# Kernel optimization log

Measured on AMD Instinct MI355X. Metric: run time of the kernel, lower is better.

Reference implementation:

```python
import jax, jax.numpy as jnp
import numpy as np

N = 100000      # nodes (categories_nums[0])
E = 1600000     # edges
FEAT = 16       # features_num
HID = 32        # hidden
IDE = 16        # id_embed_size
EMB = 8         # embed_size
CAT_MAX = 1000  # categorical vocab (categories_nums[1:])
K = 3           # TAGConv hops (sparse=False)
NC = 2          # num_class
IN_DIM = IDE + 2 * EMB + HID  # 64 -> TAGConv input
EPS = 1e-5


def layer_norm(x, g, b):
    m = jnp.mean(x, axis=-1, keepdims=True)
    v = jnp.mean((x - m) ** 2, axis=-1, keepdims=True)
    return (x - m) * jax.lax.rsqrt(v + EPS) * g + b


def setup_inputs() -> dict:
    key = jax.random.key(0)
    ks = jax.random.split(key, 20)
    s = 0.05
    return {
        "x": jax.random.normal(ks[0], (N, FEAT), jnp.float32),
        "edge_index": jax.random.randint(ks[1], (2, E), 0, N, jnp.int64),
        "edge_weight": jax.random.uniform(ks[2], (E,), jnp.float32),
        "categories_value": jax.random.randint(ks[3], (N, 3), 0, CAT_MAX, jnp.int64),
        "id_table": jax.random.normal(ks[4], (N, IDE), jnp.float32) * s,
        "lin0_id_W": jax.random.normal(ks[5], (IDE, IDE), jnp.float32) * s,
        "lin0_id_b": jnp.zeros((IDE,), jnp.float32),
        "emb1": jax.random.normal(ks[6], (CAT_MAX, EMB), jnp.float32) * s,
        "emb2": jax.random.normal(ks[7], (CAT_MAX, EMB), jnp.float32) * s,
        "lin0_emb_W": jax.random.normal(ks[8], (2 * EMB, 2 * EMB), jnp.float32) * s,
        "lin0_emb_b": jnp.zeros((2 * EMB,), jnp.float32),
        "lin0_W": jax.random.normal(ks[9], (FEAT, HID), jnp.float32) * s,
        "lin0_b": jnp.zeros((HID,), jnp.float32),
        "ln0_g": jnp.ones((IN_DIM,), jnp.float32),
        "ln0_b": jnp.zeros((IN_DIM,), jnp.float32),
        "tag_W": jax.random.normal(ks[10], (K + 1, IN_DIM, HID), jnp.float32) * s,
        "tag_b": jnp.zeros((HID,), jnp.float32),
        "ln1_g": jnp.ones((HID,), jnp.float32),
        "ln1_b": jnp.zeros((HID,), jnp.float32),
        "lin1_W": jax.random.normal(ks[11], (HID, NC), jnp.float32) * s,
        "lin1_b": jnp.zeros((NC,), jnp.float32),
    }


def reference(x, edge_index, edge_weight, categories_value, id_table, lin0_id_W,
              lin0_id_b, emb1, emb2, lin0_emb_W, lin0_emb_b, lin0_W, lin0_b,
              ln0_g, ln0_b, tag_W, tag_b, ln1_g, ln1_b, lin1_W, lin1_b):
    # eval mode: dropouts are identity
    h = jax.nn.elu(x @ lin0_W + lin0_b)                       # [N, HID]
    ide = id_table[categories_value[:, 0]]                    # [N, IDE]
    ide = jax.nn.elu(ide @ lin0_id_W + lin0_id_b)
    er = jnp.concatenate([emb1[categories_value[:, 1]],
                          emb2[categories_value[:, 2]]], axis=1)  # [N, 2*EMB]
    er = jax.nn.elu(er @ lin0_emb_W + lin0_emb_b)
    feat = jnp.concatenate([ide, h, er], axis=1)              # [N, IN_DIM]
    feat = layer_norm(feat, ln0_g, ln0_b)

    # TAGConv: gcn_norm without self-loops, K-hop propagation
    row, col = edge_index[0], edge_index[1]                   # source -> target
    deg = jax.ops.segment_sum(edge_weight, col, num_segments=N)
    dis = jnp.where(deg > 0, deg ** -0.5, 0.0)
    norm = dis[row] * edge_weight * dis[col]                  # [E]

    out = feat @ tag_W[0]                                     # [N, HID]
    xk = feat
    for k in range(1, K + 1):
        xk = jax.ops.segment_sum(xk[row] * norm[:, None], col, num_segments=N)
        out = out + xk @ tag_W[k]
    out = out + tag_b

    out = jax.nn.relu(out)
    out = layer_norm(out, ln1_g, ln1_b)
    out = out @ lin1_W + lin1_b                               # [N, NC]
    return jax.nn.log_softmax(out, axis=-1)
```

## Files before the change

kernel.cpp:

```cpp
#include <hip/hip_runtime.h>
#include <hip/hip_bf16.h>

typedef unsigned short u16;
typedef unsigned int   u32;
typedef unsigned long long u64;
typedef u32 u32x2 __attribute__((ext_vector_type(2)));
typedef u32 u32x4 __attribute__((ext_vector_type(4)));

#define FIX_SCALE 16777216.0f
#define FIX_INV   (1.0f / 16777216.0f)
#define CNT_SHIFT 40
#define DEG_MASK  ((1ULL << CNT_SHIFT) - 1)

__device__ __forceinline__ float b2f(u16 u) { return __uint_as_float(((u32)u) << 16); }
__device__ __forceinline__ u16 f2b(float f) {
    u32 u = __float_as_uint(f);
    return (u16)((u + 0x7FFFu + ((u >> 16) & 1u)) >> 16);
}
__device__ __forceinline__ float elu(float v) { return v > 0.f ? v : expm1f(v); }
__device__ __forceinline__ float ldf(const void* p, size_t i, int f32) {
    return f32 ? ((const float*)p)[i] : b2f(((const u16*)p)[i]);
}
__device__ __forceinline__ float plo(u32 a) { return __uint_as_float(a << 16); }
__device__ __forceinline__ float phi(u32 a) { return __uint_as_float(a & 0xFFFF0000u); }

__global__ void k_flags(const u32* __restrict__ gw, const int* __restrict__ ei,
                        const int* __restrict__ cat, int* __restrict__ flags) {
    if (threadIdx.x == 0 && blockIdx.x == 0) {
        flags[0] = (gw[0] == 0x3F800000u) ? 1 : 0;
        flags[1] = ((ei[1]  | ei[3]  | ei[5]  | ei[7])  == 0) ? 2 : 1;
        flags[2] = ((cat[1] | cat[3] | cat[5] | cat[7]) == 0) ? 2 : 1;
    }
}

__global__ __launch_bounds__(256) void k_feathist(
    const void* __restrict__ x, const int* __restrict__ cat,
    const void* __restrict__ id_table, const void* __restrict__ W_id, const void* __restrict__ b_id,
    const void* __restrict__ emb1, const void* __restrict__ emb2,
    const void* __restrict__ W_emb, const void* __restrict__ b_emb,
    const void* __restrict__ W0, const void* __restrict__ b0,
    const void* __restrict__ g0, const void* __restrict__ bb0,
    const void* __restrict__ tagW0,
    u32* __restrict__ feat, float* __restrict__ out_acc,
    const int* __restrict__ ei, const void* __restrict__ ew,
    u64* __restrict__ packed, u16* __restrict__ rank,
    const int* __restrict__ flags, int N, int E, int nbN)
{
    __shared__ float sW0[512];
    __shared__ float sb0[32];
    __shared__ float sWid[256];
    __shared__ float sbid[16];
    __shared__ float sWe[256];
    __shared__ float sbe[16];
    __shared__ float sg[64], sb[64];
    __shared__ float sT0t[2048];
    int tid = threadIdx.x;
    int f32 = flags[0], s = flags[1], cs = flags[2];

    int e0 = blockIdx.x * 512 + tid;
    int e1 = e0 + 256;
    u64 old0 = 0, old1 = 0;
    bool h0 = (e0 < E), h1 = (e1 < E);
    const int* colp = ei + (size_t)E * s;
    if (h0) {
        int cdst = colp[(size_t)e0 * s];
        float w = ldf(ew, e0, f32);
        old0 = atomicAdd(&packed[cdst], (1ULL << CNT_SHIFT) | (u64)(w * FIX_SCALE + 0.5f));
    }
    if (h1) {
        int cdst = colp[(size_t)e1 * s];
        float w = ldf(ew, e1, f32);
        old1 = atomicAdd(&packed[cdst], (1ULL << CNT_SHIFT) | (u64)(w * FIX_SCALE + 0.5f));
    }

    if (blockIdx.x < nbN) {
        for (int i = tid; i < 512; i += 256) sW0[i] = ldf(W0, i, f32);
        if (tid < 32) sb0[tid] = ldf(b0, tid, f32);
        sWid[tid] = ldf(W_id, tid, f32);
        if (tid < 16) sbid[tid] = ldf(b_id, tid, f32);
        sWe[tid] = ldf(W_emb, tid, f32);
        if (tid < 16) sbe[tid] = ldf(b_emb, tid, f32);
        if (tid < 64) { sg[tid] = ldf(g0, tid, f32); sb[tid] = ldf(bb0, tid, f32); }
        for (int i = tid; i < 2048; i += 256) {
            int j = i >> 6, d = i & 63;
            sT0t[i] = ldf(tagW0, (size_t)d * 32 + j, f32);
        }
        __syncthreads();

        int i = blockIdx.x * 256 + tid;
        if (i < N) {
            size_t cb = (size_t)i * 3 * cs;
            int c0 = cat[cb], c1 = cat[cb + cs], c2 = cat[cb + 2 * cs];
            float f[64];
            {
                float t[16];
                #pragma unroll
                for (int q = 0; q < 16; q++) t[q] = ldf(id_table, (size_t)c0 * 16 + q, f32);
                #pragma unroll
                for (int j = 0; j < 16; j++) {
                    float a = sbid[j];
                    #pragma unroll
                    for (int ff = 0; ff < 16; ff++) a += t[ff] * sWid[ff * 16 + j];
                    f[j] = elu(a);
                }
            }
            {
                float t[16];
                #pragma unroll
                for (int q = 0; q < 16; q++) t[q] = ldf(x, (size_t)i * 16 + q, f32);
                #pragma unroll
                for (int j = 0; j < 32; j++) {
                    float a = sb0[j];
                    #pragma unroll
                    for (int ff = 0; ff < 16; ff++) a += t[ff] * sW0[ff * 32 + j];
                    f[16 + j] = elu(a);
                }
            }
            {
                float t[16];
                #pragma unroll
                for (int q = 0; q < 8; q++) t[q] = ldf(emb1, (size_t)c1 * 8 + q, f32);
                #pragma unroll
                for (int q = 0; q < 8; q++) t[8 + q] = ldf(emb2, (size_t)c2 * 8 + q, f32);
                #pragma unroll
                for (int j = 0; j < 16; j++) {
                    float a = sbe[j];
                    #pragma unroll
                    for (int ff = 0; ff < 16; ff++) a += t[ff] * sWe[ff * 16 + j];
                    f[48 + j] = elu(a);
                }
            }
            float m = 0.f;
            #pragma unroll
            for (int d = 0; d < 64; d++) m += f[d];
            m *= (1.f / 64.f);
            float var = 0.f;
            #pragma unroll
            for (int d = 0; d < 64; d++) { float df = f[d] - m; var += df * df; }
            var *= (1.f / 64.f);
            float rs = rsqrtf(var + 1e-5f);
            #pragma unroll
            for (int d = 0; d < 64; d++) f[d] = (f[d] - m) * rs * sg[d] + sb[d];

            u32* fp = feat + (size_t)i * 32;
            #pragma unroll
            for (int q = 0; q < 32; q++) fp[q] = ((u32)f2b(f[2 * q + 1]) << 16) | f2b(f[2 * q]);

            float* oa = out_acc + (size_t)i * 32;
            for (int j = 0; j < 32; j++) {
                float a = 0.f;
                #pragma unroll
                for (int d = 0; d < 64; d++) a += f[d] * sT0t[j * 64 + d];
                oa[j] = a;
            }
        }
    }
    if (h0) rank[e0] = (u16)(old0 >> CNT_SHIFT);
    if (h1) rank[e1] = (u16)(old1 >> CNT_SHIFT);
}

__global__ __launch_bounds__(256) void k_scan1(const u64* __restrict__ packed, int* __restrict__ ebuf,
                                               int* __restrict__ bsum, float* __restrict__ dis, int N)
{
    __shared__ int sdat[256];
    int tid = threadIdx.x;
    int i = blockIdx.x * 256 + tid;
    u64 pv = (i < N) ? packed[i] : 0ULL;
    int v = (int)(pv >> CNT_SHIFT);
    sdat[tid] = v;
    __syncthreads();
    for (int off = 1; off < 256; off <<= 1) {
        int t = (tid >= off) ? sdat[tid - off] : 0;
        __syncthreads();
        sdat[tid] += t;
        __syncthreads();
    }
    if (i < N) {
        ebuf[i] = sdat[tid] - v;
        u64 db = pv & DEG_MASK;
        dis[i] = db ? rsqrtf((float)db * FIX_INV) : 0.f;
    }
    if (tid == 255) bsum[blockIdx.x] = sdat[255];
}

__global__ __launch_bounds__(512) void k_scan2(const int* __restrict__ bsum, int* __restrict__ boff, int NB)
{
    __shared__ int sdat[512];
    __shared__ int scarry;
    int tid = threadIdx.x;
    if (tid == 0) scarry = 0;
    __syncthreads();
    for (int base = 0; base < NB; base += 512) {
        int i = base + tid;
        int v = (i < NB) ? bsum[i] : 0;
        sdat[tid] = v;
        __syncthreads();
        for (int off = 1; off < 512; off <<= 1) {
            int t = (tid >= off) ? sdat[tid - off] : 0;
            __syncthreads();
            sdat[tid] += t;
            __syncthreads();
        }
        if (i < NB) boff[i] = scarry + sdat[tid] - v;
        __syncthreads();
        if (tid == 0) scarry += sdat[511];
        __syncthreads();
    }
}

__global__ __launch_bounds__(256) void k_scan3(const int* __restrict__ ebuf, const int* __restrict__ boff,
                                               int* __restrict__ rowptr, int N, int E)
{
    int i = blockIdx.x * 256 + threadIdx.x;
    if (i >= N) return;
    rowptr[i] = boff[blockIdx.x] + ebuf[i];
    if (i == N - 1) rowptr[N] = E;
}

__global__ __launch_bounds__(256) void k_scatter(const int* __restrict__ ei, const void* __restrict__ ew,
                                                 const float* __restrict__ dis, const u16* __restrict__ rank,
                                                 const int* __restrict__ rowptr, int2* __restrict__ csr,
                                                 const int* __restrict__ flags, int E)
{
    int f32 = flags[0], s = flags[1];
    const int* row = ei;
    const int* col = ei + (size_t)E * s;
    int e = blockIdx.x * 256 + threadIdx.x;
    if (e >= E) return;
    int r = row[(size_t)e * s], c = col[(size_t)e * s];
    float nrm = dis[r] * ldf(ew, e, f32) * dis[c];
    csr[rowptr[c] + (int)rank[e]] = make_int2(r, __float_as_int(nrm));
}

template<int FOLD>
__global__ __launch_bounds__(256) void k_hop(
    const u32* __restrict__ fin, u32* __restrict__ fout, float* __restrict__ oacc,
    const int* __restrict__ rowptr, const int2* __restrict__ csr,
    const void* __restrict__ tagW, const int* __restrict__ flags, int N, int k)
{
    __shared__ float sT[FOLD ? 2048 : 1];
    if (FOLD) {
        int f32 = flags[0];
        size_t tb = (size_t)k * 2048;
        for (int i = threadIdx.x; i < 2048; i += 256) sT[i] = ldf(tagW, tb + i, f32);
        __syncthreads();
    }
    int tid = threadIdx.x;
    int node = blockIdx.x * 4 + (tid >> 6);
    if (node >= N) return;
    int lane = tid & 63;
    int o = (lane >> 3) & 7;
    int c = lane & 7;
    int start = rowptr[node], end = rowptr[node + 1];

    const u32x4* fin4 = (const u32x4*)fin;
    float v0 = 0.f, v1 = 0.f, v2 = 0.f, v3 = 0.f;
    float v4 = 0.f, v5 = 0.f, v6 = 0.f, v7 = 0.f;
    int e = start;
    for (; e + 16 <= end; e += 16) {
        int2 ma = csr[e + o];
        int2 mb = csr[e + 8 + o];
        u32x4 aa = fin4[(size_t)(u32)ma.x * 8 + c];
        u32x4 ab = fin4[(size_t)(u32)mb.x * 8 + c];
        float wa = __int_as_float(ma.y), wb = __int_as_float(mb.y);
        v0 += plo(aa.x) * wa; v1 += phi(aa.x) * wa; v2 += plo(aa.y) * wa; v3 += phi(aa.y) * wa;
        v4 += plo(aa.z) * wa; v5 += phi(aa.z) * wa; v6 += plo(aa.w) * wa; v7 += phi(aa.w) * wa;
        v0 += plo(ab.x) * wb; v1 += phi(ab.x) * wb; v2 += plo(ab.y) * wb; v3 += phi(ab.y) * wb;
        v4 += plo(ab.z) * wb; v5 += phi(ab.z) * wb; v6 += plo(ab.w) * wb; v7 += phi(ab.w) * wb;
    }
    for (; e < end; e += 8) {
        int ee = e + o;
        int2 m = (ee < end) ? csr[ee] : make_int2(0, 0);
        u32x4 a = fin4[(size_t)(u32)m.x * 8 + c];
        float w = __int_as_float(m.y);
        v0 += plo(a.x) * w; v1 += phi(a.x) * w; v2 += plo(a.y) * w; v3 += phi(a.y) * w;
        v4 += plo(a.z) * w; v5 += phi(a.z) * w; v6 += plo(a.w) * w; v7 += phi(a.w) * w;
    }
    v0 += __shfl_xor(v0, 8);  v1 += __shfl_xor(v1, 8);  v2 += __shfl_xor(v2, 8);  v3 += __shfl_xor(v3, 8);
    v4 += __shfl_xor(v4, 8);  v5 += __shfl_xor(v5, 8);  v6 += __shfl_xor(v6, 8);  v7 += __shfl_xor(v7, 8);
    v0 += __shfl_xor(v0, 16); v1 += __shfl_xor(v1, 16); v2 += __shfl_xor(v2, 16); v3 += __shfl_xor(v3, 16);
    v4 += __shfl_xor(v4, 16); v5 += __shfl_xor(v5, 16); v6 += __shfl_xor(v6, 16); v7 += __shfl_xor(v7, 16);
    v0 += __shfl_xor(v0, 32); v1 += __shfl_xor(v1, 32); v2 += __shfl_xor(v2, 32); v3 += __shfl_xor(v3, 32);
    v4 += __shfl_xor(v4, 32); v5 += __shfl_xor(v5, 32); v6 += __shfl_xor(v6, 32); v7 += __shfl_xor(v7, 32);

    if (lane < 8) {
        u32x4 pw;
        pw.x = ((u32)f2b(v1) << 16) | f2b(v0);
        pw.y = ((u32)f2b(v3) << 16) | f2b(v2);
        pw.z = ((u32)f2b(v5) << 16) | f2b(v4);
        pw.w = ((u32)f2b(v7) << 16) | f2b(v6);
        ((u32x4*)fout)[(size_t)node * 8 + lane] = pw;
    }

    if (FOLD) {
        int col = lane & 31, h = lane >> 5;
        float acc = 0.f;
        #pragma unroll
        for (int q = 0; q < 4; q++) {
            int csrc = h * 4 + q;
            int d0 = csrc * 8;
            float b0 = __shfl(v0, csrc);
            float b1 = __shfl(v1, csrc);
            float b2 = __shfl(v2, csrc);
            float b3 = __shfl(v3, csrc);
            float b4 = __shfl(v4, csrc);
            float b5 = __shfl(v5, csrc);
            float b6 = __shfl(v6, csrc);
            float b7 = __shfl(v7, csrc);
            acc += b0 * sT[(d0 + 0) * 32 + col] + b1 * sT[(d0 + 1) * 32 + col]
                 + b2 * sT[(d0 + 2) * 32 + col] + b3 * sT[(d0 + 3) * 32 + col]
                 + b4 * sT[(d0 + 4) * 32 + col] + b5 * sT[(d0 + 5) * 32 + col]
                 + b6 * sT[(d0 + 6) * 32 + col] + b7 * sT[(d0 + 7) * 32 + col];
        }
        acc += __shfl_xor(acc, 32);
        if (h == 0) oacc[(size_t)node * 32 + col] += acc;
    }
}

__global__ __launch_bounds__(256) void k_head(
    const float* __restrict__ oacc, const u32* __restrict__ x2b, const u32* __restrict__ x3b,
    const void* __restrict__ tagW, const void* __restrict__ tag_b,
    const void* __restrict__ g1, const void* __restrict__ b1,
    const void* __restrict__ W1, const void* __restrict__ bb1,
    void* __restrict__ out, const int* __restrict__ flags, int N)
{
    __shared__ float sT2t[2048], sT3t[2048];
    __shared__ float stb[32], sg[32], sbb[32], sW1[64], sb1v[2];
    int tid = threadIdx.x;
    int f32 = flags[0];
    for (int i = tid; i < 2048; i += 256) {
        int j = i >> 6, d = i & 63;
        sT2t[i] = ldf(tagW, (size_t)2 * 2048 + (size_t)d * 32 + j, f32);
        sT3t[i] = ldf(tagW, (size_t)3 * 2048 + (size_t)d * 32 + j, f32);
    }
    if (tid < 32) { stb[tid] = ldf(tag_b, tid, f32); sg[tid] = ldf(g1, tid, f32); sbb[tid] = ldf(b1, tid, f32); }
    if (tid < 64) sW1[tid] = ldf(W1, tid, f32);
    if (tid < 2) sb1v[tid] = ldf(bb1, tid, f32);
    __syncthreads();

    int i = blockIdx.x * 256 + tid;
    if (i >= N) return;

    float acc[32];
    const float4* oa4 = (const float4*)(oacc + (size_t)i * 32);
    #pragma unroll
    for (int q = 0; q < 8; q++) {
        float4 t = oa4[q];
        acc[4 * q] = t.x; acc[4 * q + 1] = t.y; acc[4 * q + 2] = t.z; acc[4 * q + 3] = t.w;
    }
    float xv[64];
    {
        const u32* p = x2b + (size_t)i * 32;
        #pragma unroll
        for (int q = 0; q < 32; q++) { u32 a = p[q]; xv[2 * q] = plo(a); xv[2 * q + 1] = phi(a); }
        for (int j = 0; j < 32; j++) {
            float a = 0.f;
            #pragma unroll
            for (int d = 0; d < 64; d++) a += xv[d] * sT2t[j * 64 + d];
            acc[j] += a;
        }
    }
    {
        const u32* p = x3b + (size_t)i * 32;
        #pragma unroll
        for (int q = 0; q < 32; q++) { u32 a = p[q]; xv[2 * q] = plo(a); xv[2 * q + 1] = phi(a); }
        for (int j = 0; j < 32; j++) {
            float a = 0.f;
            #pragma unroll
            for (int d = 0; d < 64; d++) a += xv[d] * sT3t[j * 64 + d];
            acc[j] += a;
        }
    }
    float o[32]; float m = 0.f;
    #pragma unroll
    for (int j = 0; j < 32; j++) { float t = acc[j] + stb[j]; t = t > 0.f ? t : 0.f; o[j] = t; m += t; }
    m *= (1.f / 32.f);
    float var = 0.f;
    #pragma unroll
    for (int j = 0; j < 32; j++) { float d = o[j] - m; var += d * d; }
    var *= (1.f / 32.f);
    float rs = rsqrtf(var + 1e-5f);
    float z0 = sb1v[0], z1 = sb1v[1];
    #pragma unroll
    for (int j = 0; j < 32; j++) {
        float t = (o[j] - m) * rs * sg[j] + sbb[j];
        z0 += t * sW1[2 * j];
        z1 += t * sW1[2 * j + 1];
    }
    float mx = fmaxf(z0, z1);
    float l = mx + logf(expf(z0 - mx) + expf(z1 - mx));
    if (f32) {
        ((float*)out)[(size_t)i * 2]     = z0 - l;
        ((float*)out)[(size_t)i * 2 + 1] = z1 - l;
    } else {
        *((u32*)((u16*)out + (size_t)i * 2)) = ((u32)f2b(z1 - l) << 16) | f2b(z0 - l);
    }
}

extern "C" void kernel_launch(void* const* d_in, const int* in_sizes, int n_in,
                              void* d_out, int out_size, void* d_ws, size_t ws_size,
                              hipStream_t stream)
{
    const void* x        = d_in[0];
    const int*  ei       = (const int*)d_in[1];
    const void* ew       = d_in[2];
    const int*  cat      = (const int*)d_in[3];
    const void* id_table = d_in[4];
    const void* W_id     = d_in[5];
    const void* b_id     = d_in[6];
    const void* emb1     = d_in[7];
    const void* emb2     = d_in[8];
    const void* W_emb    = d_in[9];
    const void* b_emb    = d_in[10];
    const void* W0       = d_in[11];
    const void* b0       = d_in[12];
    const void* g0       = d_in[13];
    const void* bb0      = d_in[14];
    const void* tagW     = d_in[15];
    const void* tag_b    = d_in[16];
    const void* g1       = d_in[17];
    const void* b1       = d_in[18];
    const void* W1       = d_in[19];
    const void* bb1      = d_in[20];

    int N = in_sizes[0] / 16;
    int E = in_sizes[2];
    int nb = (N + 255) / 256;
    int eb = (E + 255) / 256;
    int eb2 = (E + 511) / 512;

    char* ws = (char*)d_ws;
    size_t off = 0;
    int*   flags  = (int*)(ws + off);   off += 256;
    float* oacc   = (float*)(ws + off); off += (size_t)N * 32 * 4;
    u32*   featA  = (u32*)(ws + off);   off += (size_t)N * 32 * 4;
    u32*   f1     = (u32*)(ws + off);   off += (size_t)N * 32 * 4;
    int2*  csr    = (int2*)(ws + off);  off += (size_t)E * 8;
    int*   rowptr = (int*)(ws + off);   off += ((size_t)N + 1) * 4;
    off = (off + 255) & ~(size_t)255;
    u16*   rank   = (u16*)(ws + off);   off += (size_t)E * 2;
    off = (off + 255) & ~(size_t)255;
    u64*   packed = (u64*)(ws + off);   off += (size_t)N * 8;
    int*   ebuf   = (int*)(ws + off);   off += (size_t)N * 4;
    float* dis    = (float*)(ws + off); off += (size_t)N * 4;
    int*   bsum   = (int*)(ws + off);   off += (size_t)nb * 4;
    int*   boff   = (int*)(ws + off);   off += (size_t)nb * 4;

    hipMemsetAsync(packed, 0, (size_t)N * 8, stream);
    k_flags<<<1, 64, 0, stream>>>((const u32*)g0, ei, cat, flags);

    k_feathist<<<eb2, 256, 0, stream>>>(x, cat, id_table, W_id, b_id, emb1, emb2, W_emb, b_emb,
                                        W0, b0, g0, bb0, tagW, featA, oacc,
                                        ei, ew, packed, rank, flags, N, E, nb);
    k_scan1<<<nb, 256, 0, stream>>>(packed, ebuf, bsum, dis, N);
    k_scan2<<<1, 512, 0, stream>>>(bsum, boff, nb);
    k_scan3<<<nb, 256, 0, stream>>>(ebuf, boff, rowptr, N, E);
    k_scatter<<<eb, 256, 0, stream>>>(ei, ew, dis, rank, rowptr, csr, flags, E);

    int hb = (N + 3) / 4;
    k_hop<1><<<hb, 256, 0, stream>>>(featA, f1, oacc, rowptr, csr, tagW, flags, N, 1);
    k_hop<0><<<hb, 256, 0, stream>>>(f1, featA, oacc, rowptr, csr, tagW, flags, N, 2);
    k_hop<0><<<hb, 256, 0, stream>>>(featA, f1, oacc, rowptr, csr, tagW, flags, N, 3);
    k_head<<<nb, 256, 0, stream>>>(oacc, featA, f1, tagW, tag_b, g1, b1, W1, bb1,
                                   d_out, flags, N);
}
```

Baseline: 434.0 us.

## Reassociate TAGConv with Horner form to propagate 32-wide projected features

Instead of propagating the 64-dim features three hops and projecting each hop, the feature kernel projects the normalized features by each tag weight up front (Z_k = feat·W_k, 32-wide). The hops then run in Horner form, A(A(A Z3 + Z2) + Z1), so every gather moves 32 bf16 values instead of 64 and the per-hop matmul folds disappear. This halves gather traffic in the hops and simplifies the head, at the cost of more matmul work and an 8192-float shared table in the feature kernel, which may lower its occupancy. It also changes where bf16 rounding happens.

Result: faster. 365.8 us (-15.7%).

```diff
diff --git a/kernel.cpp b/kernel.cpp
--- a/kernel.cpp
+++ b/kernel.cpp
@@ -40,8 +40,8 @@
     const void* __restrict__ W_emb, const void* __restrict__ b_emb,
     const void* __restrict__ W0, const void* __restrict__ b0,
     const void* __restrict__ g0, const void* __restrict__ bb0,
-    const void* __restrict__ tagW0,
-    u32* __restrict__ feat, float* __restrict__ out_acc,
+    const void* __restrict__ tagW,
+    float* __restrict__ out_acc, u32* __restrict__ z1, u32* __restrict__ z2, u32* __restrict__ z3,
     const int* __restrict__ ei, const void* __restrict__ ew,
     u64* __restrict__ packed, u16* __restrict__ rank,
     const int* __restrict__ flags, int N, int E, int nbN)
@@ -53,7 +53,7 @@
     __shared__ float sWe[256];
     __shared__ float sbe[16];
     __shared__ float sg[64], sb[64];
-    __shared__ float sT0t[2048];
+    __shared__ float sTt[8192];
     int tid = threadIdx.x;
     int f32 = flags[0], s = flags[1], cs = flags[2];
 
@@ -81,9 +81,9 @@
         sWe[tid] = ldf(W_emb, tid, f32);
         if (tid < 16) sbe[tid] = ldf(b_emb, tid, f32);
         if (tid < 64) { sg[tid] = ldf(g0, tid, f32); sb[tid] = ldf(bb0, tid, f32); }
-        for (int i = tid; i < 2048; i += 256) {
-            int j = i >> 6, d = i & 63;
-            sT0t[i] = ldf(tagW0, (size_t)d * 32 + j, f32);
+        for (int i = tid; i < 8192; i += 256) {
+            int k = i >> 11, r = i & 2047, j = r >> 6, d = r & 63;
+            sTt[i] = ldf(tagW, (size_t)k * 2048 + (size_t)d * 32 + j, f32);
         }
         __syncthreads();
 
@@ -142,16 +142,26 @@
             #pragma unroll
             for (int d = 0; d < 64; d++) f[d] = (f[d] - m) * rs * sg[d] + sb[d];
 
-            u32* fp = feat + (size_t)i * 32;
-            #pragma unroll
-            for (int q = 0; q < 32; q++) fp[q] = ((u32)f2b(f[2 * q + 1]) << 16) | f2b(f[2 * q]);
-
             float* oa = out_acc + (size_t)i * 32;
             for (int j = 0; j < 32; j++) {
                 float a = 0.f;
                 #pragma unroll
-                for (int d = 0; d < 64; d++) a += f[d] * sT0t[j * 64 + d];
+                for (int d = 0; d < 64; d++) a += f[d] * sTt[j * 64 + d];
                 oa[j] = a;
+            }
+            #pragma unroll
+            for (int k = 1; k <= 3; k++) {
+                u32* zp = ((k == 1) ? z1 : (k == 2) ? z2 : z3) + (size_t)i * 16;
+                const float* T = sTt + k * 2048;
+                for (int j = 0; j < 16; j++) {
+                    float a0 = 0.f, a1 = 0.f;
+                    #pragma unroll
+                    for (int d = 0; d < 64; d++) {
+                        a0 += f[d] * T[(2 * j) * 64 + d];
+                        a1 += f[d] * T[(2 * j + 1) * 64 + d];
+                    }
+                    zp[j] = ((u32)f2b(a1) << 16) | f2b(a0);
+                }
             }
         }
     }
@@ -232,19 +242,11 @@
     csr[rowptr[c] + (int)rank[e]] = make_int2(r, __float_as_int(nrm));
 }
 
-template<int FOLD>
-__global__ __launch_bounds__(256) void k_hop(
-    const u32* __restrict__ fin, u32* __restrict__ fout, float* __restrict__ oacc,
-    const int* __restrict__ rowptr, const int2* __restrict__ csr,
-    const void* __restrict__ tagW, const int* __restrict__ flags, int N, int k)
-{
-    __shared__ float sT[FOLD ? 2048 : 1];
-    if (FOLD) {
-        int f32 = flags[0];
-        size_t tb = (size_t)k * 2048;
-        for (int i = threadIdx.x; i < 2048; i += 256) sT[i] = ldf(tagW, tb + i, f32);
-        __syncthreads();
-    }
+template<int ADD>
+__global__ __launch_bounds__(256) void k_ahop(
+    const u32* __restrict__ zin, const u32* __restrict__ zadd, u32* __restrict__ uout,
+    const int* __restrict__ rowptr, const int2* __restrict__ csr, int N)
+{
     int tid = threadIdx.x;
     int node = blockIdx.x * 4 + (tid >> 6);
     if (node >= N) return;
@@ -253,86 +255,51 @@
     int c = lane & 7;
     int start = rowptr[node], end = rowptr[node + 1];
 
-    const u32x4* fin4 = (const u32x4*)fin;
+    const u32x2* fin2 = (const u32x2*)zin;
     float v0 = 0.f, v1 = 0.f, v2 = 0.f, v3 = 0.f;
-    float v4 = 0.f, v5 = 0.f, v6 = 0.f, v7 = 0.f;
     int e = start;
     for (; e + 16 <= end; e += 16) {
         int2 ma = csr[e + o];
         int2 mb = csr[e + 8 + o];
-        u32x4 aa = fin4[(size_t)(u32)ma.x * 8 + c];
-        u32x4 ab = fin4[(size_t)(u32)mb.x * 8 + c];
+        u32x2 aa = fin2[(size_t)(u32)ma.x * 8 + c];
+        u32x2 ab = fin2[(size_t)(u32)mb.x * 8 + c];
         float wa = __int_as_float(ma.y), wb = __int_as_float(mb.y);
         v0 += plo(aa.x) * wa; v1 += phi(aa.x) * wa; v2 += plo(aa.y) * wa; v3 += phi(aa.y) * wa;
-        v4 += plo(aa.z) * wa; v5 += phi(aa.z) * wa; v6 += plo(aa.w) * wa; v7 += phi(aa.w) * wa;
         v0 += plo(ab.x) * wb; v1 += phi(ab.x) * wb; v2 += plo(ab.y) * wb; v3 += phi(ab.y) * wb;
-        v4 += plo(ab.z) * wb; v5 += phi(ab.z) * wb; v6 += plo(ab.w) * wb; v7 += phi(ab.w) * wb;
     }
     for (; e < end; e += 8) {
         int ee = e + o;
         int2 m = (ee < end) ? csr[ee] : make_int2(0, 0);
-        u32x4 a = fin4[(size_t)(u32)m.x * 8 + c];
+        u32x2 a = fin2[(size_t)(u32)m.x * 8 + c];
         float w = __int_as_float(m.y);
         v0 += plo(a.x) * w; v1 += phi(a.x) * w; v2 += plo(a.y) * w; v3 += phi(a.y) * w;
-        v4 += plo(a.z) * w; v5 += phi(a.z) * w; v6 += plo(a.w) * w; v7 += phi(a.w) * w;
     }
     v0 += __shfl_xor(v0, 8);  v1 += __shfl_xor(v1, 8);  v2 += __shfl_xor(v2, 8);  v3 += __shfl_xor(v3, 8);
-    v4 += __shfl_xor(v4, 8);  v5 += __shfl_xor(v5, 8);  v6 += __shfl_xor(v6, 8);  v7 += __shfl_xor(v7, 8);
     v0 += __shfl_xor(v0, 16); v1 += __shfl_xor(v1, 16); v2 += __shfl_xor(v2, 16); v3 += __shfl_xor(v3, 16);
-    v4 += __shfl_xor(v4, 16); v5 += __shfl_xor(v5, 16); v6 += __shfl_xor(v6, 16); v7 += __shfl_xor(v7, 16);
     v0 += __shfl_xor(v0, 32); v1 += __shfl_xor(v1, 32); v2 += __shfl_xor(v2, 32); v3 += __shfl_xor(v3, 32);
-    v4 += __shfl_xor(v4, 32); v5 += __shfl_xor(v5, 32); v6 += __shfl_xor(v6, 32); v7 += __shfl_xor(v7, 32);
 
     if (lane < 8) {
-        u32x4 pw;
+        if (ADD) {
+            u32x2 z = ((const u32x2*)zadd)[(size_t)node * 8 + lane];
+            v0 += plo(z.x); v1 += phi(z.x); v2 += plo(z.y); v3 += phi(z.y);
+        }
+        u32x2 pw;
         pw.x = ((u32)f2b(v1) << 16) | f2b(v0);
         pw.y = ((u32)f2b(v3) << 16) | f2b(v2);
-        pw.z = ((u32)f2b(v5) << 16) | f2b(v4);
-        pw.w = ((u32)f2b(v7) << 16) | f2b(v6);
-        ((u32x4*)fout)[(size_t)node * 8 + lane] = pw;
-    }
-
-    if (FOLD) {
-        int col = lane & 31, h = lane >> 5;
-        float acc = 0.f;
-        #pragma unroll
-        for (int q = 0; q < 4; q++) {
-            int csrc = h * 4 + q;
-            int d0 = csrc * 8;
-            float b0 = __shfl(v0, csrc);
-            float b1 = __shfl(v1, csrc);
-            float b2 = __shfl(v2, csrc);
-            float b3 = __shfl(v3, csrc);
-            float b4 = __shfl(v4, csrc);
-            float b5 = __shfl(v5, csrc);
-            float b6 = __shfl(v6, csrc);
-            float b7 = __shfl(v7, csrc);
-            acc += b0 * sT[(d0 + 0) * 32 + col] + b1 * sT[(d0 + 1) * 32 + col]
-                 + b2 * sT[(d0 + 2) * 32 + col] + b3 * sT[(d0 + 3) * 32 + col]
-                 + b4 * sT[(d0 + 4) * 32 + col] + b5 * sT[(d0 + 5) * 32 + col]
-                 + b6 * sT[(d0 + 6) * 32 + col] + b7 * sT[(d0 + 7) * 32 + col];
-        }
-        acc += __shfl_xor(acc, 32);
-        if (h == 0) oacc[(size_t)node * 32 + col] += acc;
+        ((u32x2*)uout)[(size_t)node * 8 + lane] = pw;
     }
 }
 
 __global__ __launch_bounds__(256) void k_head(
-    const float* __restrict__ oacc, const u32* __restrict__ x2b, const u32* __restrict__ x3b,
-    const void* __restrict__ tagW, const void* __restrict__ tag_b,
+    const float* __restrict__ oacc, const u32* __restrict__ t1,
+    const void* __restrict__ tag_b,
     const void* __restrict__ g1, const void* __restrict__ b1,
     const void* __restrict__ W1, const void* __restrict__ bb1,
     void* __restrict__ out, const int* __restrict__ flags, int N)
 {
-    __shared__ float sT2t[2048], sT3t[2048];
     __shared__ float stb[32], sg[32], sbb[32], sW1[64], sb1v[2];
     int tid = threadIdx.x;
     int f32 = flags[0];
-    for (int i = tid; i < 2048; i += 256) {
-        int j = i >> 6, d = i & 63;
-        sT2t[i] = ldf(tagW, (size_t)2 * 2048 + (size_t)d * 32 + j, f32);
-        sT3t[i] = ldf(tagW, (size_t)3 * 2048 + (size_t)d * 32 + j, f32);
-    }
     if (tid < 32) { stb[tid] = ldf(tag_b, tid, f32); sg[tid] = ldf(g1, tid, f32); sbb[tid] = ldf(b1, tid, f32); }
     if (tid < 64) sW1[tid] = ldf(W1, tid, f32);
     if (tid < 2) sb1v[tid] = ldf(bb1, tid, f32);
@@ -348,28 +315,12 @@
         float4 t = oa4[q];
         acc[4 * q] = t.x; acc[4 * q + 1] = t.y; acc[4 * q + 2] = t.z; acc[4 * q + 3] = t.w;
     }
-    float xv[64];
-    {
-        const u32* p = x2b + (size_t)i * 32;
-        #pragma unroll
-        for (int q = 0; q < 32; q++) { u32 a = p[q]; xv[2 * q] = plo(a); xv[2 * q + 1] = phi(a); }
-        for (int j = 0; j < 32; j++) {
-            float a = 0.f;
-            #pragma unroll
-            for (int d = 0; d < 64; d++) a += xv[d] * sT2t[j * 64 + d];
-            acc[j] += a;
-        }
-    }
-    {
-        const u32* p = x3b + (size_t)i * 32;
-        #pragma unroll
-        for (int q = 0; q < 32; q++) { u32 a = p[q]; xv[2 * q] = plo(a); xv[2 * q + 1] = phi(a); }
-        for (int j = 0; j < 32; j++) {
-            float a = 0.f;
-            #pragma unroll
-            for (int d = 0; d < 64; d++) a += xv[d] * sT3t[j * 64 + d];
-            acc[j] += a;
-        }
+    const u32x2* tp = (const u32x2*)t1 + (size_t)i * 8;
+    #pragma unroll
+    for (int q = 0; q < 8; q++) {
+        u32x2 z = tp[q];
+        acc[4 * q]     += plo(z.x); acc[4 * q + 1] += phi(z.x);
+        acc[4 * q + 2] += plo(z.y); acc[4 * q + 3] += phi(z.y);
     }
     float o[32]; float m = 0.f;
     #pragma unroll
@@ -433,8 +384,10 @@
     size_t off = 0;
     int*   flags  = (int*)(ws + off);   off += 256;
     float* oacc   = (float*)(ws + off); off += (size_t)N * 32 * 4;
-    u32*   featA  = (u32*)(ws + off);   off += (size_t)N * 32 * 4;
-    u32*   f1     = (u32*)(ws + off);   off += (size_t)N * 32 * 4;
+    u32*   z1     = (u32*)(ws + off);   off += (size_t)N * 16 * 4;
+    u32*   z2     = (u32*)(ws + off);   off += (size_t)N * 16 * 4;
+    u32*   z3     = (u32*)(ws + off);   off += (size_t)N * 16 * 4;
+    u32*   u2     = (u32*)(ws + off);   off += (size_t)N * 16 * 4;
     int2*  csr    = (int2*)(ws + off);  off += (size_t)E * 8;
     int*   rowptr = (int*)(ws + off);   off += ((size_t)N + 1) * 4;
     off = (off + 255) & ~(size_t)255;
@@ -450,7 +403,7 @@
     k_flags<<<1, 64, 0, stream>>>((const u32*)g0, ei, cat, flags);
 
     k_feathist<<<eb2, 256, 0, stream>>>(x, cat, id_table, W_id, b_id, emb1, emb2, W_emb, b_emb,
-                                        W0, b0, g0, bb0, tagW, featA, oacc,
+                                        W0, b0, g0, bb0, tagW, oacc, z1, z2, z3,
                                         ei, ew, packed, rank, flags, N, E, nb);
     k_scan1<<<nb, 256, 0, stream>>>(packed, ebuf, bsum, dis, N);
     k_scan2<<<1, 512, 0, stream>>>(bsum, boff, nb);
@@ -458,9 +411,8 @@
     k_scatter<<<eb, 256, 0, stream>>>(ei, ew, dis, rank, rowptr, csr, flags, E);
 
     int hb = (N + 3) / 4;
-    k_hop<1><<<hb, 256, 0, stream>>>(featA, f1, oacc, rowptr, csr, tagW, flags, N, 1);
-    k_hop<0><<<hb, 256, 0, stream>>>(f1, featA, oacc, rowptr, csr, tagW, flags, N, 2);
-    k_hop<0><<<hb, 256, 0, stream>>>(featA, f1, oacc, rowptr, csr, tagW, flags, N, 3);
-    k_head<<<nb, 256, 0, stream>>>(oacc, featA, f1, tagW, tag_b, g1, b1, W1, bb1,
-                                   d_out, flags, N);
-}
+    k_ahop<1><<<hb, 256, 0, stream>>>(z3, z2, u2, rowptr, csr, N);
+    k_ahop<1><<<hb, 256, 0, stream>>>(u2, z1, z3, rowptr, csr, N);
+    k_ahop<0><<<hb, 256, 0, stream>>>(z3, z1, z2, rowptr, csr, N);
+    k_head<<<nb, 256, 0, stream>>>(oacc, z2, tag_b, g1, b1, W1, bb1, d_out, flags, N);
+}
```
